# Kernel tuning notes

Hardware: AMD Instinct MI355X
Metric: run time of the kernel (lower is better)

The kernel has to match this reference:

```python
import jax, jax.numpy as jnp
import numpy as np

N, Q, P, S, B = 262144, 256, 10, 8, 4096


def setup_inputs() -> dict:
    key = jax.random.key(0)
    k1, k2, k3, k4 = jax.random.split(key, 4)
    x = jax.random.normal(k1, (N, Q), dtype=jnp.float32)
    beta_u = jax.random.normal(k2, (Q, P, S), dtype=jnp.float32)
    beta_z = jax.random.normal(k3, (Q, P, S), dtype=jnp.float32)
    seg_ids = jnp.sort(jax.random.randint(k4, (N,), 0, B, dtype=jnp.int64))
    return {"x": x, "beta_u": beta_u, "beta_z": beta_z, "seg_ids": seg_ids,
            "num_segments": B}


def reference(x, beta_u, beta_z, seg_ids, num_segments):
    # b = sqrt(mean over feature dim of beta_z^2): [1, P, S]
    b = jnp.sqrt(jnp.mean(beta_z ** 2, axis=0, keepdims=True))
    eta = beta_z / b                                   # [Q, P, S]
    # attention logits per instance: [N, P, S]
    _w = jnp.einsum('iq,qps->ips', x, beta_u)
    # scatter_softmax over instances within each bag (dim 0)
    seg_max = jax.ops.segment_max(_w, seg_ids, num_segments=num_segments)
    ex = jnp.exp(_w - seg_max[seg_ids])
    denom = jax.ops.segment_sum(ex, seg_ids, num_segments=num_segments)
    w = ex / denom[seg_ids]                            # [N, P, S]
    t = jnp.einsum('iq,qps->ips', x, eta)              # [N, P, S]
    # weighted bag pooling (segment_add_csr equivalent): [B, P, S]
    z_bag = jax.ops.segment_sum(w * t, seg_ids, num_segments=num_segments)
    mean = jnp.mean(z_bag, axis=0)
    std = jnp.std(z_bag, axis=0, ddof=1)               # torch .std is unbiased
    std = jnp.where(jnp.isnan(std), jnp.float32(1.0), std)
    return b * (z_bag - mean) / std
```

## Files before the change

kernel.cpp:

```cpp
#include <hip/hip_runtime.h>
#include <hip/hip_bf16.h>
#include <math.h>

#define NN 262144
#define QQ 256
#define PS 80
#define BB 4096
#define NSLOT 4
#define RT 64
#define NITER 8
#define A_BYTES 4096
#define B_BYTES 10240
#define STG 14336
#define SMEM_BYTES 30720

typedef _Float16 f16x8 __attribute__((ext_vector_type(8)));
typedef float f32x4  __attribute__((ext_vector_type(4)));
typedef const __attribute__((address_space(1))) unsigned int g_u32;
typedef __attribute__((address_space(3))) unsigned int l_u32;

__device__ inline unsigned short f16b(float f) {
  return __builtin_bit_cast(unsigned short, (_Float16)f);
}
__device__ inline float f16tof(unsigned short u) {
  return (float)__builtin_bit_cast(_Float16, u);
}

__global__ void bprep_k(const float* __restrict__ bu, const float* __restrict__ bz,
                        unsigned short* __restrict__ bSwz) {
  int gid = blockIdx.x * 256 + threadIdx.x;
  if (gid >= 5120) return;
  int kt  = gid / 640;
  int rem = gid - kt * 640;
  int kg  = rem / 160;
  int c   = rem - kg * 160;
  int csw = c ^ (kg << 2);
  unsigned short* dst = bSwz + (size_t)kt * 5120 + kg * 1280 + csw * 8;
  int kbase = kt * 32 + kg * 8;
#pragma unroll
  for (int j = 0; j < 8; ++j) {
    int k = kbase + j;
    float v = (c < PS) ? bu[k * PS + c] : bz[k * PS + (c - PS)];
    dst[j] = f16b(v);
  }
}

__global__ void seg_bounds_k(const int* __restrict__ seg, int* __restrict__ segstart) {
  int b = blockIdx.x * blockDim.x + threadIdx.x;
  if (b > BB) return;
  if (b == BB) { segstart[BB] = NN; return; }
  int lo = 0, hi = NN;
  while (lo < hi) {
    int mid = (lo + hi) >> 1;
    if (seg[mid] < b) lo = mid + 1; else hi = mid;
  }
  segstart[b] = lo;
}

__global__ __launch_bounds__(256, 4) void fused_k(
    const float* __restrict__ x, const unsigned short* __restrict__ bSwz,
    const int* __restrict__ seg, const int* __restrict__ segstart,
    float* __restrict__ pm, float* __restrict__ pse, float* __restrict__ pst) {
  __shared__ __align__(16) char smem[SMEM_BYTES];
  const int tid  = threadIdx.x;
  const int wid  = tid >> 6;
  const int lane = tid & 63;
  const int rs   = blockIdx.x * RT;

  const int wr   = (wid & 1) * 32;
  const int cw   = wid >> 1;
  const int lrow = lane & 15;
  const int lk16 = lane >> 4;

  const int ra = tid >> 2;
  const int kg = tid & 3;
  const float* xp = x + (size_t)(rs + ra) * QQ + kg * 8;

  float4 xr[2][2];

#define BGLOAD(kt_, b_) do {                                                  \
    char* dstb = smem + (b_) * STG + A_BYTES;                                 \
    const char* srcb = (const char*)bSwz + (size_t)(kt_) * B_BYTES;           \
    __builtin_amdgcn_global_load_lds(                                         \
        (g_u32*)(srcb + wid * 1024 + lane * 16),                              \
        (l_u32*)(dstb + wid * 1024), 16, 0, 0);                               \
    __builtin_amdgcn_global_load_lds(                                         \
        (g_u32*)(srcb + 4096 + wid * 1024 + lane * 16),                       \
        (l_u32*)(dstb + 4096 + wid * 1024), 16, 0, 0);                        \
    if (wid < 2)                                                              \
      __builtin_amdgcn_global_load_lds(                                       \
          (g_u32*)(srcb + 8192 + wid * 1024 + lane * 16),                     \
          (l_u32*)(dstb + 8192 + wid * 1024), 16, 0, 0);                      \
  } while (0)

#define LOADI(s_, t_) do {                                                    \
    xr[s_][0] = *reinterpret_cast<const float4*>(xp + (t_) * 32);             \
    xr[s_][1] = *reinterpret_cast<const float4*>(xp + (t_) * 32 + 4);         \
  } while (0)

#define WRITEI(s_, b_) do {                                                   \
    float4 v0 = xr[s_][0], v1 = xr[s_][1];                                    \
    unsigned short a0 = f16b(v0.x), a1 = f16b(v0.y), a2 = f16b(v0.z), a3 = f16b(v0.w); \
    unsigned short a4 = f16b(v1.x), a5 = f16b(v1.y), a6 = f16b(v1.z), a7 = f16b(v1.w); \
    uint4 w = make_uint4((unsigned)a0 | ((unsigned)a1 << 16),                 \
                         (unsigned)a2 | ((unsigned)a3 << 16),                 \
                         (unsigned)a4 | ((unsigned)a5 << 16),                 \
                         (unsigned)a6 | ((unsigned)a7 << 16));                \
    *reinterpret_cast<uint4*>(smem + (b_) * STG + kg * 1024 +                 \
                              ((ra ^ (kg << 2)) * 16)) = w;                   \
  } while (0)

  f32x4 acc[2][5];
#pragma unroll
  for (int m = 0; m < 2; ++m)
#pragma unroll
    for (int n = 0; n < 5; ++n) acc[m][n] = (f32x4){0.f, 0.f, 0.f, 0.f};

  LOADI(0, 0);
  BGLOAD(0, 0);
  WRITEI(0, 0);
  LOADI(1, 1);
  __syncthreads();

#pragma unroll
  for (int t = 0; t < NITER; ++t) {
    if (t < NITER - 1) BGLOAD(t + 1, (t + 1) & 1);
    if (t < NITER - 2) LOADI(t & 1, t + 2);

    const char* A_ = smem + (t & 1) * STG;
    const char* B_ = A_ + A_BYTES;
    f16x8 ah[2];
#pragma unroll
    for (int m = 0; m < 2; ++m) {
      int r = wr + m * 16 + lrow;
      ah[m] = *reinterpret_cast<const f16x8*>(A_ + lk16 * 1024 + ((r ^ (lk16 << 2)) * 16));
    }
    __builtin_amdgcn_s_setprio(1);
#pragma unroll
    for (int n = 0; n < 5; ++n) {
      int c = cw * 80 + n * 16 + lrow;
      f16x8 bf = *reinterpret_cast<const f16x8*>(B_ + lk16 * 2560 + ((c ^ (lk16 << 2)) * 16));
      acc[0][n] = __builtin_amdgcn_mfma_f32_16x16x32_f16(ah[0], bf, acc[0][n], 0, 0, 0);
      acc[1][n] = __builtin_amdgcn_mfma_f32_16x16x32_f16(ah[1], bf, acc[1][n], 0, 0, 0);
    }
    __builtin_amdgcn_s_setprio(0);

    if (t < NITER - 1) WRITEI((t + 1) & 1, (t + 1) & 1);
    __syncthreads();
  }
#undef BGLOAD
#undef LOADI
#undef WRITEI

  float* res_u          = reinterpret_cast<float*>(smem);
  unsigned short* res_v = reinterpret_cast<unsigned short*>(smem + 20480);
#pragma unroll
  for (int m = 0; m < 2; ++m)
#pragma unroll
    for (int n = 0; n < 5; ++n)
#pragma unroll
      for (int rr = 0; rr < 4; ++rr) {
        int row = wr + m * 16 + lk16 * 4 + rr;
        int col = n * 16 + lrow;
        if (cw == 0) res_u[row * 80 + col] = acc[m][n][rr];
        else         res_v[row * 80 + col] = f16b(acc[m][n][rr]);
      }
  __syncthreads();

  int b0 = seg[rs];
  int b1 = seg[rs + RT - 1];
  int nu = (b1 - b0 + 1) * PS;
  for (int u = tid; u < nu; u += 256) {
    int bag = b0 + u / PS;
    int c   = u % PS;
    int sb  = segstart[bag];
    int lo  = max(sb, rs) - rs;
    int hi  = min(segstart[bag + 1], rs + RT) - rs;
    float m_ = -3.4e38f, se = 0.f, st = 0.f;
    for (int r = lo; r < hi; ++r) {
      float v  = res_u[r * 80 + c];
      float tv = f16tof(res_v[r * 80 + c]);
      float nm = fmaxf(m_, v);
      float sc = __expf(m_ - nm);
      float ee = __expf(v - nm);
      se = se * sc + ee;
      st = st * sc + ee * tv;
      m_ = nm;
    }
    int slot = blockIdx.x - (sb >> 6);
    size_t p = ((size_t)bag * NSLOT + slot) * PS + c;
    pm[p] = m_; pse[p] = se; pst[p] = st;
  }
}

__global__ __launch_bounds__(256) void combine_k(
    const int* __restrict__ segstart,
    const float* __restrict__ pm, const float* __restrict__ pse,
    const float* __restrict__ pst, float* __restrict__ zb) {
  int i = blockIdx.x * 256 + threadIdx.x;
  if (i >= BB * PS) return;
  int bag = i / PS, c = i % PS;
  int sb = segstart[bag], eb = segstart[bag + 1];
  float z = 0.f;
  if (eb > sb) {
    int ns = ((eb - 1) >> 6) - (sb >> 6) + 1;
    ns = min(ns, NSLOT);
    float m = -3.4e38f, se = 0.f, st = 0.f;
    for (int s = 0; s < ns; ++s) {
      size_t p = ((size_t)bag * NSLOT + s) * PS + c;
      float m2 = pm[p], se2 = pse[p], st2 = pst[p];
      float nm = fmaxf(m, m2);
      float s1 = __expf(m - nm);
      float s2 = __expf(m2 - nm);
      se = se * s1 + se2 * s2;
      st = st * s1 + st2 * s2;
      m = nm;
    }
    z = st / se;
  }
  zb[i] = z;
}

__device__ inline float wave_sum(float v) {
#pragma unroll
  for (int o = 32; o > 0; o >>= 1) v += __shfl_down(v, o, 64);
  return v;
}

__global__ __launch_bounds__(256) void finalize_k(
    const float* __restrict__ bz, float* __restrict__ zb_out) {
  const int c = blockIdx.x;
  const int t = threadIdx.x;

  float bvz = bz[t * PS + c];
  float bsq = bvz * bvz;

  float s = 0.f, ss = 0.f;
  for (int b = t; b < BB; b += 256) {
    float z = zb_out[b * PS + c];
    s += z;
    ss += z * z;
  }

  __shared__ float w0[4], w1[4], w2[4];
  float a0 = wave_sum(bsq);
  float a1 = wave_sum(s);
  float a2 = wave_sum(ss);
  int wid = t >> 6, lane = t & 63;
  if (lane == 0) { w0[wid] = a0; w1[wid] = a1; w2[wid] = a2; }
  __syncthreads();

  __shared__ float sh[3];
  if (t == 0) {
    float B0 = w0[0] + w0[1] + w0[2] + w0[3];
    float S1 = w1[0] + w1[1] + w1[2] + w1[3];
    float S2 = w2[0] + w2[1] + w2[2] + w2[3];
    float bval = sqrtf(B0 / (float)QQ);
    float mean = S1 / (float)BB;
    float var = (S2 - (float)BB * mean * mean) / (float)(BB - 1);
    float sd = sqrtf(fmaxf(var, 0.f));
    if (!(sd > 0.f) || sd != sd) sd = 1.f;
    sh[0] = bval; sh[1] = mean; sh[2] = sd;
  }
  __syncthreads();
  float bval = sh[0], mean = sh[1], sd = sh[2];
  for (int b = t; b < BB; b += 256) {
    zb_out[b * PS + c] = bval * (zb_out[b * PS + c] - mean) / sd;
  }
}

extern "C" void kernel_launch(void* const* d_in, const int* in_sizes, int n_in,
                              void* d_out, int out_size, void* d_ws, size_t ws_size,
                              hipStream_t stream) {
  const float* x   = (const float*)d_in[0];
  const float* bu  = (const float*)d_in[1];
  const float* bz  = (const float*)d_in[2];
  const int*   seg = (const int*)d_in[3];
  float* out = (float*)d_out;

  char* ws = (char*)d_ws;
  int* segstart        = (int*)ws;
  unsigned short* bSwz = (unsigned short*)(ws + 16640);
  size_t pn  = (size_t)BB * NSLOT * PS;
  float* pm  = (float*)(ws + 98560);
  float* pse = pm + pn;
  float* pst = pse + pn;

  bprep_k<<<20, 256, 0, stream>>>(bu, bz, bSwz);
  seg_bounds_k<<<(BB + 1 + 255) / 256, 256, 0, stream>>>(seg, segstart);
  fused_k<<<NN / RT, 256, 0, stream>>>(x, bSwz, seg, segstart, pm, pse, pst);
  combine_k<<<(BB * PS + 255) / 256, 256, 0, stream>>>(segstart, pm, pse, pst, out);
  finalize_k<<<PS, 256, 0, stream>>>(bz, out);
}
```

Before: 105.0 us.

## Load MFMA operands directly from global into registers, dropping LDS staging

The GEMM main loop no longer stages x and the f16 beta tile through shared memory with swizzled writes and per-iteration barriers. Each lane now reads its own MFMA A fragment straight from global as fp32, converts it to f16 in registers, and reads B fragments from an unswizzled flat buffer, double-buffered in registers. The goal is to remove LDS traffic and __syncthreads. In exchange, x rows are read redundantly by the two waves sharing a column group, global access is less coalesced, and register pressure rises, so launch bounds drop from 4 to 3 blocks per SM.

```diff
diff --git a/kernel.cpp b/kernel.cpp
--- a/kernel.cpp
+++ b/kernel.cpp
@@ -9,15 +9,10 @@
 #define NSLOT 4
 #define RT 64
 #define NITER 8
-#define A_BYTES 4096
-#define B_BYTES 10240
-#define STG 14336
 #define SMEM_BYTES 30720
 
 typedef _Float16 f16x8 __attribute__((ext_vector_type(8)));
 typedef float f32x4  __attribute__((ext_vector_type(4)));
-typedef const __attribute__((address_space(1))) unsigned int g_u32;
-typedef __attribute__((address_space(3))) unsigned int l_u32;
 
 __device__ inline unsigned short f16b(float f) {
   return __builtin_bit_cast(unsigned short, (_Float16)f);
@@ -27,15 +22,14 @@
 }
 
 __global__ void bprep_k(const float* __restrict__ bu, const float* __restrict__ bz,
-                        unsigned short* __restrict__ bSwz) {
+                        unsigned short* __restrict__ bFlat) {
   int gid = blockIdx.x * 256 + threadIdx.x;
   if (gid >= 5120) return;
   int kt  = gid / 640;
   int rem = gid - kt * 640;
   int kg  = rem / 160;
   int c   = rem - kg * 160;
-  int csw = c ^ (kg << 2);
-  unsigned short* dst = bSwz + (size_t)kt * 5120 + kg * 1280 + csw * 8;
+  unsigned short* dst = bFlat + (size_t)gid * 8;
   int kbase = kt * 32 + kg * 8;
 #pragma unroll
   for (int j = 0; j < 8; ++j) {
@@ -57,8 +51,8 @@
   segstart[b] = lo;
 }
 
-__global__ __launch_bounds__(256, 4) void fused_k(
-    const float* __restrict__ x, const unsigned short* __restrict__ bSwz,
+__global__ __launch_bounds__(256, 3) void fused_k(
+    const float* __restrict__ x, const unsigned short* __restrict__ bFlat,
     const int* __restrict__ seg, const int* __restrict__ segstart,
     float* __restrict__ pm, float* __restrict__ pse, float* __restrict__ pst) {
   __shared__ __align__(16) char smem[SMEM_BYTES];
@@ -72,85 +66,60 @@
   const int lrow = lane & 15;
   const int lk16 = lane >> 4;
 
-  const int ra = tid >> 2;
-  const int kg = tid & 3;
-  const float* xp = x + (size_t)(rs + ra) * QQ + kg * 8;
-
-  float4 xr[2][2];
-
-#define BGLOAD(kt_, b_) do {                                                  \
-    char* dstb = smem + (b_) * STG + A_BYTES;                                 \
-    const char* srcb = (const char*)bSwz + (size_t)(kt_) * B_BYTES;           \
-    __builtin_amdgcn_global_load_lds(                                         \
-        (g_u32*)(srcb + wid * 1024 + lane * 16),                              \
-        (l_u32*)(dstb + wid * 1024), 16, 0, 0);                               \
-    __builtin_amdgcn_global_load_lds(                                         \
-        (g_u32*)(srcb + 4096 + wid * 1024 + lane * 16),                       \
-        (l_u32*)(dstb + 4096 + wid * 1024), 16, 0, 0);                        \
-    if (wid < 2)                                                              \
-      __builtin_amdgcn_global_load_lds(                                       \
-          (g_u32*)(srcb + 8192 + wid * 1024 + lane * 16),                     \
-          (l_u32*)(dstb + 8192 + wid * 1024), 16, 0, 0);                      \
+  const float* xA = x + (size_t)(rs + wr + lrow) * QQ + lk16 * 8;
+  const unsigned short* bA = bFlat + ((size_t)lk16 * 160 + cw * 80 + lrow) * 8;
+
+  float4 xr[2][4];
+  f16x8  br[2][5];
+
+#define LOADA(s_, t_) do {                                                    \
+    xr[s_][0] = *reinterpret_cast<const float4*>(xA + (t_) * 32);             \
+    xr[s_][1] = *reinterpret_cast<const float4*>(xA + (t_) * 32 + 4);         \
+    xr[s_][2] = *reinterpret_cast<const float4*>(xA + 16 * QQ + (t_) * 32);   \
+    xr[s_][3] = *reinterpret_cast<const float4*>(xA + 16 * QQ + (t_) * 32 + 4); \
   } while (0)
 
-#define LOADI(s_, t_) do {                                                    \
-    xr[s_][0] = *reinterpret_cast<const float4*>(xp + (t_) * 32);             \
-    xr[s_][1] = *reinterpret_cast<const float4*>(xp + (t_) * 32 + 4);         \
+#define LOADB(s_, t_) do {                                                    \
+    _Pragma("unroll")                                                         \
+    for (int n_ = 0; n_ < 5; ++n_)                                            \
+      br[s_][n_] = *reinterpret_cast<const f16x8*>(bA + (t_) * 5120 + n_ * 128); \
   } while (0)
 
-#define WRITEI(s_, b_) do {                                                   \
-    float4 v0 = xr[s_][0], v1 = xr[s_][1];                                    \
-    unsigned short a0 = f16b(v0.x), a1 = f16b(v0.y), a2 = f16b(v0.z), a3 = f16b(v0.w); \
-    unsigned short a4 = f16b(v1.x), a5 = f16b(v1.y), a6 = f16b(v1.z), a7 = f16b(v1.w); \
-    uint4 w = make_uint4((unsigned)a0 | ((unsigned)a1 << 16),                 \
-                         (unsigned)a2 | ((unsigned)a3 << 16),                 \
-                         (unsigned)a4 | ((unsigned)a5 << 16),                 \
-                         (unsigned)a6 | ((unsigned)a7 << 16));                \
-    *reinterpret_cast<uint4*>(smem + (b_) * STG + kg * 1024 +                 \
-                              ((ra ^ (kg << 2)) * 16)) = w;                   \
-  } while (0)
-
   f32x4 acc[2][5];
 #pragma unroll
   for (int m = 0; m < 2; ++m)
 #pragma unroll
     for (int n = 0; n < 5; ++n) acc[m][n] = (f32x4){0.f, 0.f, 0.f, 0.f};
 
-  LOADI(0, 0);
-  BGLOAD(0, 0);
-  WRITEI(0, 0);
-  LOADI(1, 1);
-  __syncthreads();
+  LOADA(0, 0);
+  LOADA(1, 1);
+  LOADB(0, 0);
 
 #pragma unroll
   for (int t = 0; t < NITER; ++t) {
-    if (t < NITER - 1) BGLOAD(t + 1, (t + 1) & 1);
-    if (t < NITER - 2) LOADI(t & 1, t + 2);
-
-    const char* A_ = smem + (t & 1) * STG;
-    const char* B_ = A_ + A_BYTES;
-    f16x8 ah[2];
+    const int s = t & 1;
+    f16x8 af[2];
 #pragma unroll
     for (int m = 0; m < 2; ++m) {
-      int r = wr + m * 16 + lrow;
-      ah[m] = *reinterpret_cast<const f16x8*>(A_ + lk16 * 1024 + ((r ^ (lk16 << 2)) * 16));
-    }
+      float4 u0 = xr[s][2 * m], u1 = xr[s][2 * m + 1];
+      af[m][0] = (_Float16)u0.x; af[m][1] = (_Float16)u0.y;
+      af[m][2] = (_Float16)u0.z; af[m][3] = (_Float16)u0.w;
+      af[m][4] = (_Float16)u1.x; af[m][5] = (_Float16)u1.y;
+      af[m][6] = (_Float16)u1.z; af[m][7] = (_Float16)u1.w;
+    }
+    if (t < NITER - 2) LOADA(s, t + 2);
+    if (t < NITER - 1) LOADB((t + 1) & 1, t + 1);
+
     __builtin_amdgcn_s_setprio(1);
 #pragma unroll
     for (int n = 0; n < 5; ++n) {
-      int c = cw * 80 + n * 16 + lrow;
-      f16x8 bf = *reinterpret_cast<const f16x8*>(B_ + lk16 * 2560 + ((c ^ (lk16 << 2)) * 16));
-      acc[0][n] = __builtin_amdgcn_mfma_f32_16x16x32_f16(ah[0], bf, acc[0][n], 0, 0, 0);
-      acc[1][n] = __builtin_amdgcn_mfma_f32_16x16x32_f16(ah[1], bf, acc[1][n], 0, 0, 0);
+      acc[0][n] = __builtin_amdgcn_mfma_f32_16x16x32_f16(af[0], br[s][n], acc[0][n], 0, 0, 0);
+      acc[1][n] = __builtin_amdgcn_mfma_f32_16x16x32_f16(af[1], br[s][n], acc[1][n], 0, 0, 0);
     }
     __builtin_amdgcn_s_setprio(0);
-
-    if (t < NITER - 1) WRITEI((t + 1) & 1, (t + 1) & 1);
-    __syncthreads();
-  }
-#undef BGLOAD
-#undef LOADI
-#undef WRITEI
+  }
+#undef LOADA
+#undef LOADB
 
   float* res_u          = reinterpret_cast<float*>(smem);
   unsigned short* res_v = reinterpret_cast<unsigned short*>(smem + 20480);
@@ -279,16 +248,16 @@
   float* out = (float*)d_out;
 
   char* ws = (char*)d_ws;
-  int* segstart        = (int*)ws;
-  unsigned short* bSwz = (unsigned short*)(ws + 16640);
+  int* segstart         = (int*)ws;
+  unsigned short* bFlat = (unsigned short*)(ws + 16640);
   size_t pn  = (size_t)BB * NSLOT * PS;
   float* pm  = (float*)(ws + 98560);
   float* pse = pm + pn;
   float* pst = pse + pn;
 
-  bprep_k<<<20, 256, 0, stream>>>(bu, bz, bSwz);
+  bprep_k<<<20, 256, 0, stream>>>(bu, bz, bFlat);
   seg_bounds_k<<<(BB + 1 + 255) / 256, 256, 0, stream>>>(seg, segstart);
-  fused_k<<<NN / RT, 256, 0, stream>>>(x, bSwz, seg, segstart, pm, pse, pst);
+  fused_k<<<NN / RT, 256, 0, stream>>>(x, bFlat, seg, segstart, pm, pse, pst);
   combine_k<<<(BB * PS + 255) / 256, 256, 0, stream>>>(segstart, pm, pse, pst, out);
   finalize_k<<<PS, 256, 0, stream>>>(bz, out);
 }
```

Result: slower. 137.9 us (+31.3%).
